# Kernel optimization log

Measured on AMD Instinct MI355X. Metric: run time of the kernel, lower is better.

## Reference

```python
import jax, jax.numpy as jnp
import numpy as np

EPS = 1e-6

def _silu(x):
    return x * jax.nn.sigmoid(x)

def setup_inputs() -> dict:
    key = jax.random.key(0)
    ks = jax.random.split(key, 6)
    T, B, D, N = 2048, 16, 1024, 64
    scale = (6.0 / (N + D)) ** 0.5  # xavier_uniform bound
    x = jax.random.normal(ks[0], (T, B, D), dtype=jnp.float32)
    S0 = jnp.zeros((B, N, N), dtype=jnp.float32)
    W_k = jax.random.uniform(ks[1], (N, D), minval=-scale, maxval=scale, dtype=jnp.float32)
    W_v = jax.random.uniform(ks[2], (N, D), minval=-scale, maxval=scale, dtype=jnp.float32)
    W_q = jax.random.uniform(ks[3], (N, D), minval=-scale, maxval=scale, dtype=jnp.float32)
    W_beta = jax.random.uniform(ks[4], (N, D), minval=-scale, maxval=scale, dtype=jnp.float32)
    b_beta = jnp.full((N,), 2.0, dtype=jnp.float32)
    return {"x": x, "S0": S0, "W_k": W_k, "W_v": W_v, "W_q": W_q, "W_beta": W_beta, "b_beta": b_beta}

def reference(x, S0, W_k, W_v, W_q, W_beta, b_beta):
    # x: [T, B, D] -> projections [T, B, n]
    k_all = jnp.einsum('tbd,nd->tbn', x, W_k)
    v_all = jnp.einsum('tbd,nd->tbn', x, W_v)
    q_all = jnp.einsum('tbd,nd->tbn', x, W_q)
    beta_all = jax.nn.sigmoid(jnp.einsum('tbd,nd->tbn', x, W_beta) + b_beta)

    def step(S, inp):
        k, v, q, beta = inp  # each [B, n]
        k_norm = k / (jnp.linalg.norm(k, axis=-1, keepdims=True) + EPS)
        retrieved = jnp.einsum('bij,bj->bi', S, k_norm)
        delta = v - retrieved
        outer = jnp.einsum('bi,bj->bij', delta, k_norm)
        S_new = jnp.tanh(beta[:, :, None] * S + outer)
        Sq = jnp.einsum('bij,bj->bi', S_new, q)
        out = Sq * _silu(Sq)
        return S_new, out

    S_final, output = jax.lax.scan(step, S0, (k_all, v_all, q_all, beta_all))
    return output, S_final
```

## Files before the change

### kernel.cpp

```cpp
#include <hip/hip_runtime.h>
#include <math.h>
#include <stdint.h>

#define T_DIM 2048
#define B_DIM 16
#define D_DIM 1024
#define N_DIM 64
#define EPSV 1e-6f

#define NT 256

#define TWO_LOG2E 2.885390081777927f
#define LOG2E     1.4426950408889634f

__device__ __forceinline__ float fast_rcp(float x) {
    return __builtin_amdgcn_rcpf(x);
}
__device__ __forceinline__ float sigmoid_fast(float x) {
    return fast_rcp(1.f + __builtin_amdgcn_exp2f(-LOG2E * x));
}
__device__ __forceinline__ float tanh_from_scaled(float xs) {
    float e = __builtin_amdgcn_exp2f(xs);
    return 1.f - 2.f * fast_rcp(e + 1.f);
}

template<int CTRL>
__device__ __forceinline__ float dpp_radd(float x) {
    int y = __builtin_amdgcn_update_dpp(0, __float_as_int(x), CTRL, 0xf, 0xf, true);
    return x + __int_as_float(y);
}
__device__ __forceinline__ float reduce16(float x) {
    x = dpp_radd<0xB1>(x);
    x = dpp_radd<0x4E>(x);
    x = dpp_radd<0x124>(x);
    x = dpp_radd<0x128>(x);
    return x;
}

__device__ __forceinline__ void dma16(const float* g, float* l) {
    __builtin_amdgcn_global_load_lds((const __attribute__((address_space(1))) void*)g,
                                     (__attribute__((address_space(3))) void*)l, 16, 0, 0);
}

typedef __bf16 bf16x8_t __attribute__((ext_vector_type(8)));
typedef float  f32x16_t __attribute__((ext_vector_type(16)));

union FragU { uint32_t u[4]; bf16x8_t v; };

#define BM 128
#define BK 32

__device__ __forceinline__ void load_frag_pair(const float* __restrict__ tile,
                                               int row, int s,
                                               bf16x8_t& hi, bf16x8_t& lo)
{
    const int sw = row & 7;
    const float4 f0 = *(const float4*)(tile + row * BK + 4 * (s ^ sw));
    const float4 f1 = *(const float4*)(tile + row * BK + 4 * ((s + 1) ^ sw));
    float f[8] = {f0.x, f0.y, f0.z, f0.w, f1.x, f1.y, f1.z, f1.w};
    FragU h, l;
    #pragma unroll
    for (int j = 0; j < 4; ++j) {
        uint32_t u0 = __float_as_uint(f[2 * j]);
        uint32_t u1 = __float_as_uint(f[2 * j + 1]);
        h.u[j] = (u1 & 0xffff0000u) | (u0 >> 16);
        float r0 = f[2 * j]     - __uint_as_float(u0 & 0xffff0000u);
        float r1 = f[2 * j + 1] - __uint_as_float(u1 & 0xffff0000u);
        l.u[j] = (__float_as_uint(r1) & 0xffff0000u) | (__float_as_uint(r0) >> 16);
    }
    hi = h.v; lo = l.v;
}

__global__ __launch_bounds__(256) void proj_gemm_mfma(
    const float* __restrict__ x,
    const float* __restrict__ Wk, const float* __restrict__ Wv,
    const float* __restrict__ Wq, const float* __restrict__ Wb,
    const float* __restrict__ bb,
    float* __restrict__ proj)
{
    __shared__ float As[2][BM * BK];
    __shared__ float Bs[2][NT * BK];

    const int tid  = threadIdx.x;
    const int w    = tid >> 6;
    const int lane = tid & 63;
    const int m0   = blockIdx.x * BM;

    const int lrow8 = lane >> 3;
    const int lslot = (lane & 7) ^ lrow8;

    const int wm = w >> 1, wn = w & 1;
    const int cl = lane & 31;
    const int kh = lane >> 5;

    f32x16_t acc[2][4] = {};

    auto stage = [&](int buf, int kb) {
        #pragma unroll
        for (int i = 0; i < 4; ++i) {
            const int rb = w * 32 + i * 8;
            const int m  = rb + lrow8;
            dma16(x + (size_t)(m0 + m) * D_DIM + kb + 4 * lslot, &As[buf][rb * BK]);
        }
        #pragma unroll
        for (int i = 0; i < 8; ++i) {
            const int rb = w * 64 + i * 8;
            const int n  = rb + lrow8;
            const float* Wsrc = (n < 64) ? Wk : (n < 128) ? Wv : (n < 192) ? Wq : Wb;
            dma16(Wsrc + (size_t)(n & 63) * D_DIM + kb + 4 * lslot, &Bs[buf][rb * BK]);
        }
    };

    auto compute = [&](int buf) {
        const float* At = As[buf];
        const float* Bt = Bs[buf];
        #pragma unroll
        for (int ksub = 0; ksub < 2; ++ksub) {
            const int s = ksub * 4 + kh * 2;
            bf16x8_t ah[2], al[2], bh[4], bl[4];
            #pragma unroll
            for (int tm = 0; tm < 2; ++tm)
                load_frag_pair(At, wm * 64 + tm * 32 + cl, s, ah[tm], al[tm]);
            #pragma unroll
            for (int tn = 0; tn < 4; ++tn)
                load_frag_pair(Bt, wn * 128 + tn * 32 + cl, s, bh[tn], bl[tn]);
            #pragma unroll
            for (int tm = 0; tm < 2; ++tm)
                #pragma unroll
                for (int tn = 0; tn < 4; ++tn) {
                    acc[tm][tn] = __builtin_amdgcn_mfma_f32_32x32x16_bf16(ah[tm], bh[tn], acc[tm][tn], 0, 0, 0);
                    acc[tm][tn] = __builtin_amdgcn_mfma_f32_32x32x16_bf16(ah[tm], bl[tn], acc[tm][tn], 0, 0, 0);
                    acc[tm][tn] = __builtin_amdgcn_mfma_f32_32x32x16_bf16(al[tm], bh[tn], acc[tm][tn], 0, 0, 0);
                }
        }
    };

    stage(0, 0);
    int cur = 0;
    for (int ks = 0; ks < D_DIM / BK; ++ks) {
        __syncthreads();
        if (ks + 1 < D_DIM / BK) stage(cur ^ 1, (ks + 1) * BK);
        compute(cur);
        cur ^= 1;
    }

    #pragma unroll
    for (int tn = 0; tn < 4; ++tn) {
        const int gcol = wn * 128 + tn * 32 + cl;
        const bool isbeta = (gcol >= 192);
        const float bias = isbeta ? bb[gcol - 192] : 0.f;
        #pragma unroll
        for (int tm = 0; tm < 2; ++tm) {
            #pragma unroll
            for (int r = 0; r < 16; ++r) {
                const int rowin = (r & 3) + 8 * (r >> 2) + 4 * kh;
                const size_t grow = (size_t)(m0 + wm * 64 + tm * 32 + rowin);
                float v = acc[tm][tn][r];
                if (isbeta) v = sigmoid_fast(v + bias);
                proj[grow * NT + gcol] = v;
            }
        }
    }
}

__global__ __launch_bounds__(256) void knorm_kernel(float* __restrict__ proj)
{
    const int w = (int)((blockIdx.x * blockDim.x + threadIdx.x) >> 6);
    const int lane = threadIdx.x & 63;
    float k = proj[(size_t)w * NT + lane];
    float s = k * k;
    #pragma unroll
    for (int off = 32; off; off >>= 1) s += __shfl_xor(s, off, 64);
    proj[(size_t)w * NT + lane] = k * fast_rcp(sqrtf(s) + EPSV);
}

__device__ __forceinline__ void step_body(float4& s, const float4 kn, const float4 q,
                                          const float vC, const float beC,
                                          int sp, int l, float& ysel)
{
    float y2 = (s.x * kn.x + s.y * kn.y) + (s.z * kn.z + s.w * kn.w);
    y2 = reduce16(y2);
    const float dC = fmaf(-TWO_LOG2E, y2, vC);
    const float bsx = beC * s.x, bsy = beC * s.y;
    const float bsz = beC * s.z, bsw = beC * s.w;
    s.x = tanh_from_scaled(fmaf(dC, kn.x, bsx));
    s.y = tanh_from_scaled(fmaf(dC, kn.y, bsy));
    s.z = tanh_from_scaled(fmaf(dC, kn.z, bsz));
    s.w = tanh_from_scaled(fmaf(dC, kn.w, bsw));
    float y1 = (s.x * q.x + s.y * q.y) + (s.z * q.z + s.w * q.w);
    y1 = reduce16(y1);
    ysel = (l == sp) ? y1 : ysel;
}

__device__ __forceinline__ void phase16(const float (*buf)[256], int t0,
                                        float4& s, int l, int i, int b,
                                        float* __restrict__ out)
{
    const float* s0 = &buf[0][0];
    const float* s1 = &buf[1][0];
    float4 kn0 = *(const float4*)(s0 + 4 * l);
    float4 q0  = *(const float4*)(s0 + 128 + 4 * l);
    float  vC0 = s0[64 + i] * TWO_LOG2E;
    float  beC0= s0[192 + i] * TWO_LOG2E;
    float4 kn1 = *(const float4*)(s1 + 4 * l);
    float4 q1  = *(const float4*)(s1 + 128 + 4 * l);
    float  vC1 = s1[64 + i] * TWO_LOG2E;
    float  beC1= s1[192 + i] * TWO_LOG2E;

    float ysel = 0.f;
    for (int j = 0; j < 8; ++j) {
        const int sp = 2 * j;
        const int p2 = (sp + 2 < 16) ? sp + 2 : 15;
        const int p3 = (sp + 3 < 16) ? sp + 3 : 15;
        const float* sA = &buf[p2][0];
        const float* sB = &buf[p3][0];
        float4 knA = *(const float4*)(sA + 4 * l);
        float4 qA  = *(const float4*)(sA + 128 + 4 * l);
        float  vCA = sA[64 + i] * TWO_LOG2E;
        float  beCA= sA[192 + i] * TWO_LOG2E;
        float4 knB = *(const float4*)(sB + 4 * l);
        float4 qB  = *(const float4*)(sB + 128 + 4 * l);
        float  vCB = sB[64 + i] * TWO_LOG2E;
        float  beCB= sB[192 + i] * TWO_LOG2E;

        step_body(s, kn0, q0, vC0, beC0, sp,     l, ysel);
        step_body(s, kn1, q1, vC1, beC1, sp + 1, l, ysel);

        kn0 = knA; q0 = qA; vC0 = vCA; beC0 = beCA;
        kn1 = knB; q1 = qB; vC1 = vCB; beC1 = beCB;
    }
    const float w = ysel;
    out[(size_t)(t0 + l) * (B_DIM * N_DIM) + b * 64 + i] = w * w * sigmoid_fast(w);
}

__global__ __launch_bounds__(128, 1) void recur6_kernel(
    const float* __restrict__ proj,
    const float* __restrict__ S0,
    float* __restrict__ out)
{
    __shared__ float bufA[16][256];
    __shared__ float bufB[16][256];

    const int wid  = blockIdx.x;
    const int wv   = threadIdx.x >> 6;
    const int lane = threadIdx.x & 63;
    const int l = lane & 15;
    const int r = lane >> 4;
    const int b = wid >> 4;
    const int i = ((wid & 15) << 2) + r;

    if (wv == 1) {
        #pragma unroll
        for (int j = 0; j < 16; ++j)
            dma16(proj + ((size_t)j * B_DIM + b) * NT + 4 * lane, &bufA[j][0]);
        __syncthreads();
        for (int t0 = 0; t0 < T_DIM; t0 += 32) {
            #pragma unroll
            for (int j = 0; j < 16; ++j) {
                int row = t0 + 16 + j; if (row > T_DIM - 1) row = T_DIM - 1;
                dma16(proj + ((size_t)row * B_DIM + b) * NT + 4 * lane, &bufB[j][0]);
            }
            __syncthreads();
            #pragma unroll
            for (int j = 0; j < 16; ++j) {
                int row = t0 + 32 + j; if (row > T_DIM - 1) row = T_DIM - 1;
                dma16(proj + ((size_t)row * B_DIM + b) * NT + 4 * lane, &bufA[j][0]);
            }
            __syncthreads();
        }
    } else {
        float4 s = *(const float4*)(S0 + ((size_t)(b * 64 + i) << 6) + 4 * l);
        __syncthreads();
        for (int t0 = 0; t0 < T_DIM; t0 += 32) {
            phase16(bufA, t0, s, l, i, b, out);
            __syncthreads();
            phase16(bufB, t0 + 16, s, l, i, b, out);
            __syncthreads();
        }
        *(float4*)(out + (size_t)T_DIM * B_DIM * N_DIM +
                   ((size_t)(b * 64 + i) << 6) + 4 * l) = s;
    }
}

extern "C" void kernel_launch(void* const* d_in, const int* in_sizes, int n_in,
                              void* d_out, int out_size, void* d_ws, size_t ws_size,
                              hipStream_t stream) {
    const float* x  = (const float*)d_in[0];
    const float* S0 = (const float*)d_in[1];
    const float* Wk = (const float*)d_in[2];
    const float* Wv = (const float*)d_in[3];
    const float* Wq = (const float*)d_in[4];
    const float* Wb = (const float*)d_in[5];
    const float* bb = (const float*)d_in[6];
    float* out  = (float*)d_out;
    float* proj = (float*)d_ws;

    proj_gemm_mfma<<<dim3(32768 / BM), dim3(256), 0, stream>>>(x, Wk, Wv, Wq, Wb, bb, proj);
    knorm_kernel<<<dim3((32768 * 64) / 256), dim3(256), 0, stream>>>(proj);
    recur6_kernel<<<dim3(256), dim3(128), 0, stream>>>(proj, S0, out);
}
```

Before: 523.4 us.

## Presplit weights to fp16 hi/lo once and convert x tiles once per block

Adds a prep kernel that splits the weights into fp16 hi/lo pairs in workspace, so the GEMM reads them directly from global memory instead of re-splitting per fragment. The GEMM drops to 64-row tiles with each wave owning 64 output columns. Each x tile is converted to fp16 hi/lo once in shared memory, behind a two-deep DMA prefetch. This removes redundant split work and shared-memory traffic for W, but adds a launch and makes every block stream W from global/L2. Switching from bf16 to fp16 splits changes rounding and may overflow for large-magnitude inputs.

```diff
diff --git a/kernel.cpp b/kernel.cpp
--- a/kernel.cpp
+++ b/kernel.cpp
@@ -12,6 +12,10 @@
 
 #define TWO_LOG2E 2.885390081777927f
 #define LOG2E     1.4426950408889634f
+
+typedef _Float16 half8 __attribute__((ext_vector_type(8)));
+typedef float    f32x16_t __attribute__((ext_vector_type(16)));
+union F4H8 { float4 f; half8 h; };
 
 __device__ __forceinline__ float fast_rcp(float x) {
     return __builtin_amdgcn_rcpf(x);
@@ -42,119 +46,136 @@
                                      (__attribute__((address_space(3))) void*)l, 16, 0, 0);
 }
 
-typedef __bf16 bf16x8_t __attribute__((ext_vector_type(8)));
-typedef float  f32x16_t __attribute__((ext_vector_type(16)));
-
-union FragU { uint32_t u[4]; bf16x8_t v; };
-
-#define BM 128
-#define BK 32
-
-__device__ __forceinline__ void load_frag_pair(const float* __restrict__ tile,
-                                               int row, int s,
-                                               bf16x8_t& hi, bf16x8_t& lo)
-{
-    const int sw = row & 7;
-    const float4 f0 = *(const float4*)(tile + row * BK + 4 * (s ^ sw));
-    const float4 f1 = *(const float4*)(tile + row * BK + 4 * ((s + 1) ^ sw));
+__global__ __launch_bounds__(256) void wprep_kernel(
+    const float* __restrict__ Wk, const float* __restrict__ Wv,
+    const float* __restrict__ Wq, const float* __restrict__ Wb,
+    float4* __restrict__ w2)
+{
+    const int c  = threadIdx.x;
+    const int k8 = blockIdx.x;
+    const float* Wsrc = (c < 64) ? Wk : (c < 128) ? Wv : (c < 192) ? Wq : Wb;
+    const float4* src = (const float4*)(Wsrc + (size_t)(c & 63) * D_DIM + k8 * 8);
+    const float4 f0 = src[0], f1 = src[1];
     float f[8] = {f0.x, f0.y, f0.z, f0.w, f1.x, f1.y, f1.z, f1.w};
-    FragU h, l;
+    F4H8 hi, lo;
     #pragma unroll
-    for (int j = 0; j < 4; ++j) {
-        uint32_t u0 = __float_as_uint(f[2 * j]);
-        uint32_t u1 = __float_as_uint(f[2 * j + 1]);
-        h.u[j] = (u1 & 0xffff0000u) | (u0 >> 16);
-        float r0 = f[2 * j]     - __uint_as_float(u0 & 0xffff0000u);
-        float r1 = f[2 * j + 1] - __uint_as_float(u1 & 0xffff0000u);
-        l.u[j] = (__float_as_uint(r1) & 0xffff0000u) | (__float_as_uint(r0) >> 16);
-    }
-    hi = h.v; lo = l.v;
-}
+    for (int j = 0; j < 8; ++j) {
+        _Float16 h = (_Float16)f[j];
+        hi.h[j] = h;
+        lo.h[j] = (_Float16)(f[j] - (float)h);
+    }
+    w2[(size_t)(2 * k8)     * 256 + c] = hi.f;
+    w2[(size_t)(2 * k8 + 1) * 256 + c] = lo.f;
+}
+
+#define BM 64
 
 __global__ __launch_bounds__(256) void proj_gemm_mfma(
     const float* __restrict__ x,
-    const float* __restrict__ Wk, const float* __restrict__ Wv,
-    const float* __restrict__ Wq, const float* __restrict__ Wb,
+    const float4* __restrict__ w2,
     const float* __restrict__ bb,
     float* __restrict__ proj)
 {
-    __shared__ float As[2][BM * BK];
-    __shared__ float Bs[2][NT * BK];
+    __shared__ float  As32[2][BM * 32];
+    __shared__ float4 Ahl[2][BM * 8];
 
     const int tid  = threadIdx.x;
     const int w    = tid >> 6;
     const int lane = tid & 63;
     const int m0   = blockIdx.x * BM;
-
-    const int lrow8 = lane >> 3;
-    const int lslot = (lane & 7) ^ lrow8;
-
-    const int wm = w >> 1, wn = w & 1;
-    const int cl = lane & 31;
-    const int kh = lane >> 5;
-
-    f32x16_t acc[2][4] = {};
-
-    auto stage = [&](int buf, int kb) {
-        #pragma unroll
-        for (int i = 0; i < 4; ++i) {
-            const int rb = w * 32 + i * 8;
-            const int m  = rb + lrow8;
-            dma16(x + (size_t)(m0 + m) * D_DIM + kb + 4 * lslot, &As[buf][rb * BK]);
-        }
-        #pragma unroll
-        for (int i = 0; i < 8; ++i) {
-            const int rb = w * 64 + i * 8;
-            const int n  = rb + lrow8;
-            const float* Wsrc = (n < 64) ? Wk : (n < 128) ? Wv : (n < 192) ? Wq : Wb;
-            dma16(Wsrc + (size_t)(n & 63) * D_DIM + kb + 4 * lslot, &Bs[buf][rb * BK]);
+    const int cl   = lane & 31;
+    const int kh   = lane >> 5;
+
+    f32x16_t acc[2][2] = {};
+
+    auto stage = [&](int buf, int t) {
+        #pragma unroll
+        for (int i = 0; i < 2; ++i) {
+            const int rb    = w * 16 + i * 8;
+            const int row   = rb + (lane >> 3);
+            const int sslot = (lane & 7) ^ ((lane >> 3) & 7);
+            dma16(x + (size_t)(m0 + row) * D_DIM + 32 * t + 4 * sslot,
+                  &As32[buf][rb * 32]);
         }
     };
-
-    auto compute = [&](int buf) {
-        const float* At = As[buf];
-        const float* Bt = Bs[buf];
-        #pragma unroll
-        for (int ksub = 0; ksub < 2; ++ksub) {
-            const int s = ksub * 4 + kh * 2;
-            bf16x8_t ah[2], al[2], bh[4], bl[4];
-            #pragma unroll
-            for (int tm = 0; tm < 2; ++tm)
-                load_frag_pair(At, wm * 64 + tm * 32 + cl, s, ah[tm], al[tm]);
-            #pragma unroll
-            for (int tn = 0; tn < 4; ++tn)
-                load_frag_pair(Bt, wn * 128 + tn * 32 + cl, s, bh[tn], bl[tn]);
+    auto convert = [&](int bs, int bd) {
+        const int row = tid >> 2, c = tid & 3, sw = row & 7;
+        const float4* s32 = (const float4*)&As32[bs][0];
+        const float4 fA = s32[row * 8 + ((2 * c)     ^ sw)];
+        const float4 fB = s32[row * 8 + ((2 * c + 1) ^ sw)];
+        float f[8] = {fA.x, fA.y, fA.z, fA.w, fB.x, fB.y, fB.z, fB.w};
+        F4H8 hi, lo;
+        #pragma unroll
+        for (int j = 0; j < 8; ++j) {
+            _Float16 h = (_Float16)f[j];
+            hi.h[j] = h;
+            lo.h[j] = (_Float16)(f[j] - (float)h);
+        }
+        Ahl[bd][row * 8 + ((2 * c)     ^ sw)] = hi.f;
+        Ahl[bd][row * 8 + ((2 * c + 1) ^ sw)] = lo.f;
+    };
+
+    stage(0, 0);
+    stage(1, 1);
+    __syncthreads();
+    convert(0, 0);
+    __syncthreads();
+
+    for (int t = 0; t < 32; ++t) {
+        if (t + 2 < 32) stage(t & 1, t + 2);
+
+        half8 bh[2][2], bl[2][2];
+        #pragma unroll
+        for (int ks = 0; ks < 2; ++ks) {
+            const int ksg = 2 * t + ks;
+            #pragma unroll
+            for (int tn = 0; tn < 2; ++tn) {
+                const int col = w * 64 + tn * 32 + cl;
+                F4H8 th, tl;
+                th.f = w2[(size_t)(4 * ksg + 2 * kh)     * 256 + col];
+                tl.f = w2[(size_t)(4 * ksg + 2 * kh + 1) * 256 + col];
+                bh[ks][tn] = th.h; bl[ks][tn] = tl.h;
+            }
+        }
+
+        if (t + 1 < 32) convert((t + 1) & 1, (t + 1) & 1);
+
+        const float4* At = &Ahl[t & 1][0];
+        #pragma unroll
+        for (int ks = 0; ks < 2; ++ks) {
+            half8 ah[2], al[2];
+            #pragma unroll
+            for (int tm = 0; tm < 2; ++tm) {
+                const int row = tm * 32 + cl;
+                const int sw  = row & 7;
+                F4H8 th, tl;
+                th.f = At[row * 8 + ((4 * ks + 2 * kh)     ^ sw)];
+                tl.f = At[row * 8 + ((4 * ks + 2 * kh + 1) ^ sw)];
+                ah[tm] = th.h; al[tm] = tl.h;
+            }
             #pragma unroll
             for (int tm = 0; tm < 2; ++tm)
                 #pragma unroll
-                for (int tn = 0; tn < 4; ++tn) {
-                    acc[tm][tn] = __builtin_amdgcn_mfma_f32_32x32x16_bf16(ah[tm], bh[tn], acc[tm][tn], 0, 0, 0);
-                    acc[tm][tn] = __builtin_amdgcn_mfma_f32_32x32x16_bf16(ah[tm], bl[tn], acc[tm][tn], 0, 0, 0);
-                    acc[tm][tn] = __builtin_amdgcn_mfma_f32_32x32x16_bf16(al[tm], bh[tn], acc[tm][tn], 0, 0, 0);
+                for (int tn = 0; tn < 2; ++tn) {
+                    acc[tm][tn] = __builtin_amdgcn_mfma_f32_32x32x16_f16(ah[tm], bh[ks][tn], acc[tm][tn], 0, 0, 0);
+                    acc[tm][tn] = __builtin_amdgcn_mfma_f32_32x32x16_f16(ah[tm], bl[ks][tn], acc[tm][tn], 0, 0, 0);
+                    acc[tm][tn] = __builtin_amdgcn_mfma_f32_32x32x16_f16(al[tm], bh[ks][tn], acc[tm][tn], 0, 0, 0);
                 }
         }
-    };
-
-    stage(0, 0);
-    int cur = 0;
-    for (int ks = 0; ks < D_DIM / BK; ++ks) {
         __syncthreads();
-        if (ks + 1 < D_DIM / BK) stage(cur ^ 1, (ks + 1) * BK);
-        compute(cur);
-        cur ^= 1;
     }
 
     #pragma unroll
-    for (int tn = 0; tn < 4; ++tn) {
-        const int gcol = wn * 128 + tn * 32 + cl;
+    for (int tn = 0; tn < 2; ++tn) {
+        const int  gcol   = w * 64 + tn * 32 + cl;
         const bool isbeta = (gcol >= 192);
-        const float bias = isbeta ? bb[gcol - 192] : 0.f;
+        const float bias  = isbeta ? bb[gcol - 192] : 0.f;
         #pragma unroll
         for (int tm = 0; tm < 2; ++tm) {
             #pragma unroll
             for (int r = 0; r < 16; ++r) {
                 const int rowin = (r & 3) + 8 * (r >> 2) + 4 * kh;
-                const size_t grow = (size_t)(m0 + wm * 64 + tm * 32 + rowin);
+                const size_t grow = (size_t)(m0 + tm * 32 + rowin);
                 float v = acc[tm][tn][r];
                 if (isbeta) v = sigmoid_fast(v + bias);
                 proj[grow * NT + gcol] = v;
@@ -294,8 +315,10 @@
     const float* bb = (const float*)d_in[6];
     float* out  = (float*)d_out;
     float* proj = (float*)d_ws;
-
-    proj_gemm_mfma<<<dim3(32768 / BM), dim3(256), 0, stream>>>(x, Wk, Wv, Wq, Wb, bb, proj);
+    float4* w2  = (float4*)((char*)d_ws + (size_t)32768 * 256 * 4);
+
+    wprep_kernel<<<dim3(128), dim3(256), 0, stream>>>(Wk, Wv, Wq, Wb, w2);
+    proj_gemm_mfma<<<dim3(32768 / BM), dim3(256), 0, stream>>>(x, w2, bb, proj);
     knorm_kernel<<<dim3((32768 * 64) / 256), dim3(256), 0, stream>>>(proj);
     recur6_kernel<<<dim3(256), dim3(128), 0, stream>>>(proj, S0, out);
 }
```

Result: faster. 470.1 us (-10.2%).
